# Kernel tuning notes

Measured on AMD Instinct MI355X. Metric: run time of the kernel, lower is better.

The kernel has to match this reference:

```python
import jax, jax.numpy as jnp
import numpy as np

N = 10000   # nodes
B = 32      # batch (hardcoded in source)
E = 40000   # edges per graph
H = 4       # attention heads
D = 10      # out_feats per head (hardcoded 10 in source)
T = 10      # GAT input feature size (hardcoded 10)
L = 2       # n_align_layers
NEG = 0.2   # LeakyReLU slope


def _leaky(z):
    return jnp.where(z >= 0, z, NEG * z)


def _ln(t):
    # LayerNorm((N,B,D), elementwise_affine=False): normalize over the whole tensor
    m = t.mean()
    v = ((t - m) ** 2).mean()
    return (t - m) * jax.lax.rsqrt(v + 1e-5)


def _gat(feat, fc_w, a_l, a_r, src, dst):
    # feat: (N,B,T); fc_w: (H*D,T); a_l,a_r: (H,D); src,dst: (E,)
    ft = jnp.einsum('nbf,of->nbo', feat, fc_w).reshape(N, B, H, D)
    el = jnp.einsum('nbhd,hd->nbh', ft, a_l)   # (N,B,H)
    er = jnp.einsum('nbhd,hd->nbh', ft, a_r)
    e = _leaky(el[src] + er[dst])              # (E,B,H)
    emax = jax.ops.segment_max(e, dst, num_segments=N)
    ee = jnp.exp(e - emax[dst])
    a = ee / jax.ops.segment_sum(ee, dst, num_segments=N)[dst]  # edge softmax per dst
    out = jax.ops.segment_sum(ft[src] * a[..., None], dst, num_segments=N)  # (N,B,H,D)
    return _leaky(out)  # activation = leaky_relu in source


def setup_inputs():
    key = jax.random.key(0)
    ks = iter(jax.random.split(key, 40))
    x = jax.random.normal(next(ks), (T, N, B, 3), dtype=jnp.float32)
    idx = lambda: jax.random.randint(next(ks), (E,), 0, N, dtype=jnp.int32)
    inp = {'x': x, 'ps_src': idx(), 'ps_dst': idx(), 'rl_src': idx(), 'rl_dst': idx()}
    def gat_params(name):
        inp[name + '_fc'] = jax.random.normal(next(ks), (L, H * D, T), dtype=jnp.float32) * 0.3
        inp[name + '_al'] = jax.random.normal(next(ks), (L, H, D), dtype=jnp.float32) * 0.3
        inp[name + '_ar'] = jax.random.normal(next(ks), (L, H, D), dtype=jnp.float32) * 0.3
    for nm in ('mu_p', 'sg_p', 'mu_r', 'sg_r'):
        gat_params(nm)
    inp['reg_mu_w'] = jax.random.normal(next(ks), (1, T), dtype=jnp.float32) * 0.3
    inp['reg_mu_b'] = jnp.zeros((1,), dtype=jnp.float32)
    inp['reg_sg_w'] = jax.random.normal(next(ks), (1, T), dtype=jnp.float32) * 0.3
    inp['reg_sg_b'] = jnp.zeros((1,), dtype=jnp.float32)
    return inp


def reference(x, mu_p_fc, mu_p_al, mu_p_ar, sg_p_fc, sg_p_al, sg_p_ar,
              mu_r_fc, mu_r_al, mu_r_ar, sg_r_fc, sg_r_al, sg_r_ar,
              reg_mu_w, reg_mu_b, reg_sg_w, reg_sg_b,
              ps_src, ps_dst, rl_src, rl_dst):
    # mode='align1' path of Net.forward
    h = jnp.transpose(x, (1, 2, 0, 3))[..., :3]  # (N,B,T,3)
    mu = h[..., 0]      # (N,B,T)
    sigma = h[..., 1]
    mu_r0, sg_r0 = mu, sigma
    # pseudo-graph alignment stack
    mu_p, sg_p = mu, sigma
    for i in range(L - 1):
        mu_p = _ln(_gat(mu_p, mu_p_fc[i], mu_p_al[i], mu_p_ar[i], ps_src, ps_dst).mean(-2))
        sg_p = _ln(_gat(sg_p, sg_p_fc[i], sg_p_al[i], sg_p_ar[i], ps_src, ps_dst).mean(-2))
        h_p = (mu_p + sg_p) / 2
        mu_p, sg_p = h_p, h_p
    # real-graph alignment stack
    mu_rl, sg_rl = mu, sigma
    for i in range(L - 1):
        mu_rl = _ln(_gat(mu_rl, mu_r_fc[i], mu_r_al[i], mu_r_ar[i], rl_src, rl_dst).mean(-2))
        sg_rl = _ln(_gat(sg_rl, sg_r_fc[i], sg_r_al[i], sg_r_ar[i], rl_src, rl_dst).mean(-2))
        h_rl = (mu_rl + sg_rl) / 2
        mu_rl, sg_rl = h_rl, h_rl
    mu_r = mu_r0 @ reg_mu_w.T + reg_mu_b                                        # (N,B,1)
    mu_pf = _gat(h_p, mu_p_fc[-1], mu_p_al[-1], mu_p_ar[-1], ps_src, ps_dst).mean(-2)
    mu_rf = _gat(h_rl, mu_r_fc[-1], mu_r_al[-1], mu_r_ar[-1], rl_src, rl_dst).mean(-2)
    sg_r = sg_r0 @ reg_sg_w.T + reg_sg_b
    sg_pf = _gat(h_p, sg_p_fc[-1], sg_p_al[-1], sg_p_ar[-1], ps_src, ps_dst).mean(-2)
    sg_rf = _gat(h_rl, sg_r_fc[-1], sg_r_al[-1], sg_r_ar[-1], rl_src, rl_dst).mean(-2)
    return ((mu_r + mu_pf + mu_rf) / 3, (sg_r + sg_pf + sg_rf) / 3)
```

## Files before the change

### kernel.cpp

```cpp
#include <hip/hip_runtime.h>
#include <hip/hip_fp16.h>


#define NN 10000
#define BB 32
#define EE 40000
#define HH 4
#define DD 10
#define TT 10
#define NEG 0.2f

#define NB   (NN*BB)
#define NBT  (NN*BB*TT)
#define BSUB 2
#define NGRP (NN*BSUB)


__device__ __forceinline__ float2 cvt2(unsigned u) {
    return __half22float2(*reinterpret_cast<const __half2*>(&u));
}
__device__ __forceinline__ void unpA(const uint4& u0, const uint4& u1, float (&fa)[10]) {
    float2 t;
    t = cvt2(u0.x); fa[0] = t.x; fa[1] = t.y;
    t = cvt2(u0.y); fa[2] = t.x; fa[3] = t.y;
    t = cvt2(u0.z); fa[4] = t.x; fa[5] = t.y;
    t = cvt2(u0.w); fa[6] = t.x; fa[7] = t.y;
    t = cvt2(u1.x); fa[8] = t.x; fa[9] = t.y;
}
__device__ __forceinline__ void unpB(const uint4& u1, const uint4& u2, float (&fb)[10]) {
    float2 t;
    t = cvt2(u1.z); fb[0] = t.x; fb[1] = t.y;
    t = cvt2(u1.w); fb[2] = t.x; fb[3] = t.y;
    t = cvt2(u2.x); fb[4] = t.x; fb[5] = t.y;
    t = cvt2(u2.y); fb[6] = t.x; fb[7] = t.y;
    t = cvt2(u2.z); fb[8] = t.x; fb[9] = t.y;
}

__global__ void extract_kernel(const float* __restrict__ x,
                               const float* __restrict__ wmu, const float* __restrict__ bmu,
                               const float* __restrict__ wsg, const float* __restrict__ bsg,
                               __half* __restrict__ msH,
                               float* __restrict__ regmu, float* __restrict__ regsg) {
    int i = blockIdx.x * blockDim.x + threadIdx.x;
    if (i >= NB) return;
    int n = i / BB, b = i % BB;
    float smu = 0.f, ssg = 0.f;
    float muv[TT], sgv[TT];
#pragma unroll
    for (int t = 0; t < TT; t++) {
        size_t xi = (((size_t)t * NN + n) * BB + b) * 3;
        float m = x[xi], s = x[xi + 1];
        muv[t] = m; sgv[t] = s;
        smu += m * wmu[t];
        ssg += s * wsg[t];
    }
    __half2* dst = (__half2*)(msH + (size_t)i * 24);
    dst[0] = __floats2half2_rn(muv[0], muv[1]);
    dst[1] = __floats2half2_rn(muv[2], muv[3]);
    dst[2] = __floats2half2_rn(muv[4], muv[5]);
    dst[3] = __floats2half2_rn(muv[6], muv[7]);
    dst[4] = __floats2half2_rn(muv[8], muv[9]);
    dst[5] = __floats2half2_rn(0.f, 0.f);
    dst[6] = __floats2half2_rn(sgv[0], sgv[1]);
    dst[7] = __floats2half2_rn(sgv[2], sgv[3]);
    dst[8] = __floats2half2_rn(sgv[4], sgv[5]);
    dst[9] = __floats2half2_rn(sgv[6], sgv[7]);
    dst[10] = __floats2half2_rn(sgv[8], sgv[9]);
    dst[11] = __floats2half2_rn(0.f, 0.f);
    regmu[i] = smu + bmu[0];
    regsg[i] = ssg + bsg[0];
}

__global__ void deg2_kernel(const int* __restrict__ dst0, int* __restrict__ deg0,
                            const int* __restrict__ dst1, int* __restrict__ deg1) {
    int e = blockIdx.x * blockDim.x + threadIdx.x;
    const int* dst = blockIdx.y ? dst1 : dst0;
    int* deg       = blockIdx.y ? deg1 : deg0;
    if (e < EE) atomicAdd(&deg[dst[e]], 1);
}

__global__ void scan2_kernel(const int* __restrict__ deg0, int* __restrict__ off0,
                             const int* __restrict__ deg1, int* __restrict__ off1) {
    const int* __restrict__ deg = blockIdx.x ? deg1 : deg0;
    int* __restrict__ off       = blockIdx.x ? off1 : off0;
    __shared__ int sm[16];
    __shared__ int carry_s;
    int tid = threadIdx.x;
    int lane = tid & 63, wid = tid >> 6;
    if (tid == 0) { carry_s = 0; off[0] = 0; }
    __syncthreads();
    for (int base = 0; base < NN; base += 1024) {
        int i = base + tid;
        int v = (i < NN) ? deg[i] : 0;
        int x = v;
#pragma unroll
        for (int s = 1; s < 64; s <<= 1) {
            int t = __shfl_up(x, s, 64);
            if (lane >= s) x += t;
        }
        if (lane == 63) sm[wid] = x;
        __syncthreads();
        if (wid == 0) {
            int w = (lane < 16) ? sm[lane] : 0;
#pragma unroll
            for (int s = 1; s < 16; s <<= 1) {
                int t = __shfl_up(w, s, 64);
                if (lane >= s) w += t;
            }
            if (lane < 16) sm[lane] = w;
        }
        __syncthreads();
        int add = carry_s + ((wid > 0) ? sm[wid - 1] : 0);
        if (i < NN) off[i + 1] = add + x;
        int total = sm[15];
        __syncthreads();
        if (tid == 0) carry_s += total;
        __syncthreads();
    }
}

__global__ void fill2_kernel(const int* __restrict__ src0, const int* __restrict__ dst0,
                             const int* __restrict__ off0, int* __restrict__ cur0,
                             int* __restrict__ csr0,
                             const int* __restrict__ src1, const int* __restrict__ dst1,
                             const int* __restrict__ off1, int* __restrict__ cur1,
                             int* __restrict__ csr1) {
    int e = blockIdx.x * blockDim.x + threadIdx.x;
    const int* src = blockIdx.y ? src1 : src0;
    const int* dst = blockIdx.y ? dst1 : dst0;
    const int* off = blockIdx.y ? off1 : off0;
    int* cursor    = blockIdx.y ? cur1 : cur0;
    int* csr       = blockIdx.y ? csr1 : csr0;
    if (e < EE) {
        int d = dst[e];
        int p = atomicAdd(&cursor[d], 1);
        csr[off[d] + p] = src[e];
    }
}

__global__ void hist2_kernel(const int* __restrict__ deg0, const int* __restrict__ deg1,
                             int* __restrict__ hist) {
    __shared__ int lh[64];
    if (threadIdx.x < 64) lh[threadIdx.x] = 0;
    __syncthreads();
    int n = blockIdx.x * blockDim.x + threadIdx.x;
    int g = blockIdx.y;
    const int* deg = g ? deg1 : deg0;
    if (n < NN) {
        int d = deg[n];
        int bin = 63 - ((d < 63) ? d : 63);
        atomicAdd(&lh[bin], 1);
    }
    __syncthreads();
    if (threadIdx.x < 64 && lh[threadIdx.x])
        atomicAdd(&hist[g * 64 + threadIdx.x], lh[threadIdx.x]);
}

__global__ void binoff_kernel(const int* __restrict__ hist, int* __restrict__ boff) {
    int g = threadIdx.x >> 6, lane = threadIdx.x & 63;
    int v = hist[g * 64 + lane];
    int x = v;
#pragma unroll
    for (int s = 1; s < 64; s <<= 1) {
        int t = __shfl_up(x, s, 64);
        if (lane >= s) x += t;
    }
    boff[g * 64 + lane] = x - v;
}

__global__ void permfill2_kernel(const int* __restrict__ deg0, const int* __restrict__ deg1,
                                 const int* __restrict__ boff, int* __restrict__ bcur,
                                 int* __restrict__ perm0, int* __restrict__ perm1) {
    __shared__ int lh[64], lbase[64];
    if (threadIdx.x < 64) lh[threadIdx.x] = 0;
    __syncthreads();
    int n = blockIdx.x * blockDim.x + threadIdx.x;
    int g = blockIdx.y;
    const int* deg = g ? deg1 : deg0;
    int* perm      = g ? perm1 : perm0;
    int bin = 0, myp = 0;
    if (n < NN) {
        int d = deg[n];
        bin = 63 - ((d < 63) ? d : 63);
        myp = atomicAdd(&lh[bin], 1);
    }
    __syncthreads();
    if (threadIdx.x < 64) {
        int c = lh[threadIdx.x];
        lbase[threadIdx.x] = c ? atomicAdd(&bcur[g * 64 + threadIdx.x], c) : 0;
    }
    __syncthreads();
    if (n < NN) perm[boff[g * 64 + bin] + lbase[bin] + myp] = n;
}

__global__ void vpre_kernel(const float* __restrict__ fc0, const float* __restrict__ al0, const float* __restrict__ ar0,
                            const float* __restrict__ fc1, const float* __restrict__ al1, const float* __restrict__ ar1,
                            const float* __restrict__ fc2, const float* __restrict__ al2, const float* __restrict__ ar2,
                            const float* __restrict__ fc3, const float* __restrict__ al3, const float* __restrict__ ar3,
                            float* __restrict__ vbuf) {
    int j = threadIdx.x;
    if (j >= 320) return;
    int g = j / 40, r = j % 40;
    int h = r / 10, t = r % 10;
    int which = g & 3, layer = g >> 2;
    const float* fc; const float* al; const float* ar;
    if (which == 0)      { fc = fc0; al = al0; ar = ar0; }
    else if (which == 1) { fc = fc1; al = al1; ar = ar1; }
    else if (which == 2) { fc = fc2; al = al2; ar = ar2; }
    else                 { fc = fc3; al = al3; ar = ar3; }
    fc += layer * (HH * DD * TT);
    al += layer * (HH * DD);
    ar += layer * (HH * DD);
    float vl = 0.f, vr = 0.f;
#pragma unroll
    for (int d = 0; d < DD; d++) {
        float w = fc[(h * DD + d) * TT + t];
        vl += al[h * DD + d] * w;
        vr += ar[h * DD + d] * w;
    }
    vbuf[g * 80 + r] = vl;
    vbuf[g * 80 + 40 + r] = vr;
}

struct PairCfg {
    const __half* f;
    const float* WA; const float* WB;
    const float* vA; const float* vB;
    const int* off; const int* csr; const int* perm;
    float* gA; float* gB;
    float* statsA; float* statsB;
};
struct PairCfg2 { PairCfg c[2]; };

__device__ __forceinline__ void eacc(const float (&fa)[TT], bool val,
                                     const float* __restrict__ v,
                                     const float (&er)[HH],
                                     float (&den)[HH], float (&acc)[HH][TT]) {
#pragma unroll
    for (int h = 0; h < HH; h++) {
        float e = 0.f;
#pragma unroll
        for (int t = 0; t < TT; t++) e += v[h * TT + t] * fa[t];
        float z = e + er[h];
        z = (z >= 0.f) ? z : NEG * z;
        float w = val ? __expf(z) : 0.f;
        den[h] += w;
#pragma unroll
        for (int t = 0; t < TT; t++) acc[h][t] += w * fa[t];
    }
}

template <bool DUALF, bool STATS>
__global__ void __launch_bounds__(256)
gatpair_kernel(PairCfg2 cfgs) {
    const PairCfg cfg = cfgs.c[blockIdx.y];
    __shared__ __align__(16) float sWA[HH * DD * 12];
    __shared__ __align__(16) float sWB[HH * DD * 12];
    for (int kk = threadIdx.x; kk < HH * DD * TT; kk += blockDim.x) {
        int r = kk / TT, t = kk - r * TT;
        sWA[r * 12 + t] = cfg.WA[kk];
        sWB[r * 12 + t] = cfg.WB[kk];
    }
    __syncthreads();

    const __half* __restrict__ f  = cfg.f;
    const int*   __restrict__ csr = cfg.csr;
    const float* __restrict__ vA  = cfg.vA;
    const float* __restrict__ vB  = cfg.vB;
    const int LDR = DUALF ? 24 : 16;

    int i = blockIdx.x * blockDim.x + threadIdx.x;
    float lsA = 0.f, lqA = 0.f, lsB = 0.f, lqB = 0.f;
    if (i < NB) {
        int bgrp = i / NGRP;
        int r = i - bgrp * NGRP;
        int slot = r >> 1;
        int b = (bgrp << 1) | (r & 1);
        int n = cfg.perm[slot];
        int nb = n * BB + b;
        int s0 = cfg.off[n], s1 = cfg.off[n + 1];

        float erA[HH], erB[HH];
        {
            const uint4* p = (const uint4*)(f + (size_t)nb * LDR);
            float fsA[TT], fsB[TT];
            if (DUALF) {
                uint4 u0 = p[0], u1 = p[1], u2 = p[2];
                unpA(u0, u1, fsA); unpB(u1, u2, fsB);
            } else {
                uint4 u0 = p[0], u1 = p[1];
                unpA(u0, u1, fsA);
#pragma unroll
                for (int t = 0; t < TT; t++) fsB[t] = fsA[t];
            }
#pragma unroll
            for (int h = 0; h < HH; h++) {
                float ea = 0.f, eb = 0.f;
#pragma unroll
                for (int t = 0; t < TT; t++) {
                    ea += vA[HH * TT + h * TT + t] * fsA[t];
                    eb += vB[HH * TT + h * TT + t] * fsB[t];
                }
                erA[h] = ea; erB[h] = eb;
            }
        }

        float accA[HH][TT], accB[HH][TT];
        float denA[HH], denB[HH];
#pragma unroll
        for (int h = 0; h < HH; h++) {
            denA[h] = 0.f; denB[h] = 0.f;
#pragma unroll
            for (int t = 0; t < TT; t++) { accA[h][t] = 0.f; accB[h][t] = 0.f; }
        }

        for (int k = s0; k < s1; k += 4) {
            int k1 = (k + 1 < s1) ? k + 1 : s0;
            int k2 = (k + 2 < s1) ? k + 2 : s0;
            int k3 = (k + 3 < s1) ? k + 3 : s0;
            bool v1 = (k + 1 < s1), v2 = (k + 2 < s1), v3 = (k + 3 < s1);
            int e0 = csr[k], e1 = csr[k1], e2 = csr[k2], e3 = csr[k3];
            const uint4* q0 = (const uint4*)(f + (size_t)(e0 * BB + b) * LDR);
            const uint4* q1 = (const uint4*)(f + (size_t)(e1 * BB + b) * LDR);
            const uint4* q2 = (const uint4*)(f + (size_t)(e2 * BB + b) * LDR);
            const uint4* q3 = (const uint4*)(f + (size_t)(e3 * BB + b) * LDR);
            if (DUALF) {
                uint4 a0 = q0[0], a1 = q0[1], a2 = q0[2];
                uint4 b0 = q1[0], b1 = q1[1], b2 = q1[2];
                uint4 c0 = q2[0], c1 = q2[1], c2 = q2[2];
                uint4 d0 = q3[0], d1 = q3[1], d2 = q3[2];
                float fa[TT], fb[TT];
                unpA(a0, a1, fa); unpB(a1, a2, fb);
                eacc(fa, true, vA, erA, denA, accA); eacc(fb, true, vB, erB, denB, accB);
                unpA(b0, b1, fa); unpB(b1, b2, fb);
                eacc(fa, v1, vA, erA, denA, accA);   eacc(fb, v1, vB, erB, denB, accB);
                unpA(c0, c1, fa); unpB(c1, c2, fb);
                eacc(fa, v2, vA, erA, denA, accA);   eacc(fb, v2, vB, erB, denB, accB);
                unpA(d0, d1, fa); unpB(d1, d2, fb);
                eacc(fa, v3, vA, erA, denA, accA);   eacc(fb, v3, vB, erB, denB, accB);
            } else {
                uint4 a0 = q0[0], a1 = q0[1];
                uint4 b0 = q1[0], b1 = q1[1];
                uint4 c0 = q2[0], c1 = q2[1];
                uint4 d0 = q3[0], d1 = q3[1];
                float fa[TT];
                unpA(a0, a1, fa);
                eacc(fa, true, vA, erA, denA, accA); eacc(fa, true, vB, erB, denB, accB);
                unpA(b0, b1, fa);
                eacc(fa, v1, vA, erA, denA, accA);   eacc(fa, v1, vB, erB, denB, accB);
                unpA(c0, c1, fa);
                eacc(fa, v2, vA, erA, denA, accA);   eacc(fa, v2, vB, erB, denB, accB);
                unpA(d0, d1, fa);
                eacc(fa, v3, vA, erA, denA, accA);   eacc(fa, v3, vB, erB, denB, accB);
            }
        }

        bool nz = (s1 > s0);
        float* gpA = cfg.gA + (size_t)nb * DD;
        float* gpB = cfg.gB + (size_t)nb * DD;

#pragma unroll
        for (int g = 0; g < 2; g++) {
            const float (*acc)[TT] = g ? accB : accA;
            const float* den = g ? denB : denA;
            const float* sW  = g ? sWB : sWA;
            float* gp        = g ? gpB : gpA;
            float rd[HH];
#pragma unroll
            for (int h = 0; h < HH; h++) rd[h] = nz ? (1.0f / den[h]) : 0.f;
            float outv[DD];
#pragma unroll
            for (int d = 0; d < DD; d++) outv[d] = 0.f;
#pragma unroll
            for (int h = 0; h < HH; h++) {
#pragma unroll
                for (int d = 0; d < DD; d++) {
                    const float* wr = &sW[(h * DD + d) * 12];
                    float4 w0 = *(const float4*)wr;
                    float4 w1 = *(const float4*)(wr + 4);
                    float2 w2 = *(const float2*)(wr + 8);
                    float va = w0.x * acc[h][0] + w0.y * acc[h][1] + w0.z * acc[h][2] + w0.w * acc[h][3]
                             + w1.x * acc[h][4] + w1.y * acc[h][5] + w1.z * acc[h][6] + w1.w * acc[h][7]
                             + w2.x * acc[h][8] + w2.y * acc[h][9];
                    va *= rd[h];
                    va = (va >= 0.f) ? va : NEG * va;
                    outv[d] += va * 0.25f;
                }
            }
#pragma unroll
            for (int d = 0; d < DD; d += 2)
                *(float2*)(gp + d) = make_float2(outv[d], outv[d + 1]);
            if (STATS) {
                float s = 0.f, q = 0.f;
#pragma unroll
                for (int d = 0; d < DD; d++) { s += outv[d]; q += outv[d] * outv[d]; }
                if (g) { lsB = s; lqB = q; } else { lsA = s; lqA = q; }
            }
        }
    }
    if (STATS) {
#pragma unroll
        for (int o = 32; o > 0; o >>= 1) {
            lsA += __shfl_down(lsA, o, 64);
            lqA += __shfl_down(lqA, o, 64);
            lsB += __shfl_down(lsB, o, 64);
            lqB += __shfl_down(lqB, o, 64);
        }
        __shared__ float ss[4][4];
        int wid = threadIdx.x >> 6, lid = threadIdx.x & 63;
        if (lid == 0) { ss[wid][0] = lsA; ss[wid][1] = lqA; ss[wid][2] = lsB; ss[wid][3] = lqB; }
        __syncthreads();
        if (threadIdx.x == 0) {
            float a0 = 0.f, a1 = 0.f, a2 = 0.f, a3 = 0.f;
#pragma unroll
            for (int w = 0; w < 4; w++) { a0 += ss[w][0]; a1 += ss[w][1]; a2 += ss[w][2]; a3 += ss[w][3]; }
            atomicAdd(&cfg.statsA[0], a0);
            atomicAdd(&cfg.statsA[1], a1);
            atomicAdd(&cfg.statsB[0], a2);
            atomicAdd(&cfg.statsB[1], a3);
        }
    }
}

__global__ void lncomb2_kernel(const float* __restrict__ gA, const float* __restrict__ gB,
                               const float* __restrict__ gA2, const float* __restrict__ gB2,
                               const float* __restrict__ stats,
                               __half* __restrict__ hp, __half* __restrict__ hrl) {
    int i = blockIdx.x * blockDim.x + threadIdx.x;
    if (i >= NB * 8) return;
    const float* ga = blockIdx.y ? gA2 : gA;
    const float* gb = blockIdx.y ? gB2 : gB;
    const float* st = stats + (blockIdx.y ? 4 : 0);
    __half2* h      = (__half2*)(blockIdx.y ? hrl : hp);
    int nb = i >> 3, t2 = i & 7;
    float v0 = 0.f, v1 = 0.f;
    if (t2 < 5) {
        const float M = (float)NBT;
        float ma = st[0] / M; float va = st[1] / M - ma * ma;
        float mb = st[2] / M; float vb = st[3] / M - mb * mb;
        float ra = rsqrtf(va + 1e-5f), rb = rsqrtf(vb + 1e-5f);
        size_t base = (size_t)nb * DD + t2 * 2;
        v0 = 0.5f * ((ga[base] - ma) * ra + (gb[base] - mb) * rb);
        v1 = 0.5f * ((ga[base + 1] - ma) * ra + (gb[base + 1] - mb) * rb);
    }
    h[(size_t)nb * 8 + t2] = __floats2half2_rn(v0, v1);
}

__global__ void outcomb2_kernel(const float* __restrict__ regmu, const float* __restrict__ regsg,
                                const float* __restrict__ gA, const float* __restrict__ gA2,
                                const float* __restrict__ gB, const float* __restrict__ gB2,
                                float* __restrict__ out) {
    int i = blockIdx.x * blockDim.x + threadIdx.x;
    if (i >= NBT) return;
    int nb = i / DD;
    if (blockIdx.y == 0) out[i]       = (regmu[nb] + gA[i] + gA2[i]) * (1.0f / 3.0f);
    else                 out[NBT + i] = (regsg[nb] + gB[i] + gB2[i]) * (1.0f / 3.0f);
}

extern "C" void kernel_launch(void* const* d_in, const int* in_sizes, int n_in,
                              void* d_out, int out_size, void* d_ws, size_t ws_size,
                              hipStream_t stream) {
    const float* x      = (const float*)d_in[0];
    const int* ps_src   = (const int*)d_in[1];
    const int* ps_dst   = (const int*)d_in[2];
    const int* rl_src   = (const int*)d_in[3];
    const int* rl_dst   = (const int*)d_in[4];
    const float* mu_p_fc = (const float*)d_in[5];
    const float* mu_p_al = (const float*)d_in[6];
    const float* mu_p_ar = (const float*)d_in[7];
    const float* sg_p_fc = (const float*)d_in[8];
    const float* sg_p_al = (const float*)d_in[9];
    const float* sg_p_ar = (const float*)d_in[10];
    const float* mu_r_fc = (const float*)d_in[11];
    const float* mu_r_al = (const float*)d_in[12];
    const float* mu_r_ar = (const float*)d_in[13];
    const float* sg_r_fc = (const float*)d_in[14];
    const float* sg_r_al = (const float*)d_in[15];
    const float* sg_r_ar = (const float*)d_in[16];
    const float* reg_mu_w = (const float*)d_in[17];
    const float* reg_mu_b = (const float*)d_in[18];
    const float* reg_sg_w = (const float*)d_in[19];
    const float* reg_sg_b = (const float*)d_in[20];

    float* out = (float*)d_out;

    float* fw = (float*)d_ws;
    __half* msH  = (__half*)fw;     fw += NB * 12;
    __half* hpH  = (__half*)fw;     fw += NB * 8;
    __half* hrlH = (__half*)fw;     fw += NB * 8;
    float* gA    = fw;              fw += NBT;
    float* gB    = fw;              fw += NBT;
    float* gA2   = fw;              fw += NBT;
    float* gB2   = fw;              fw += NBT;
    float* regmu = fw;              fw += NB;
    float* regsg = fw;              fw += NB;
    float* vbuf  = fw;              fw += 8 * 80;
    int* iw = (int*)fw;
    int* ps_off = iw;               iw += NN + 1;
    int* rl_off = iw;               iw += NN + 1;
    int* ps_csr = iw;               iw += EE;
    int* rl_csr = iw;               iw += EE;
    int* perm_ps = iw;              iw += NN;
    int* perm_rl = iw;              iw += NN;
    int* boff   = iw;               iw += 128;
    int* deg_ps = iw;               iw += NN;
    int* cur_ps = iw;               iw += NN;
    int* deg_rl = iw;               iw += NN;
    int* cur_rl = iw;               iw += NN;
    int* hist   = iw;               iw += 128;
    int* bcur   = iw;               iw += 128;
    float* stats = (float*)iw;
    size_t zero_bytes = (size_t)(4 * NN + 256) * sizeof(int) + 8 * sizeof(float);
    hipMemsetAsync(deg_ps, 0, zero_bytes, stream);

    const int TPB = 256;
    const int GRID_NB  = (NB + TPB - 1) / TPB;
    const int GRID_NBT = (NBT + TPB - 1) / TPB;
    const int GRID_LN  = (NB * 8 + TPB - 1) / TPB;
    const int GRID_E   = (EE + TPB - 1) / TPB;
    const int GRID_N   = (NN + TPB - 1) / TPB;

    extract_kernel<<<GRID_NB, TPB, 0, stream>>>(x, reg_mu_w, reg_mu_b, reg_sg_w, reg_sg_b,
                                                msH, regmu, regsg);

    {
        dim3 g(GRID_E, 2, 1);
        dim3 gn(GRID_N, 2, 1);
        deg2_kernel<<<g, TPB, 0, stream>>>(ps_dst, deg_ps, rl_dst, deg_rl);
        scan2_kernel<<<2, 1024, 0, stream>>>(deg_ps, ps_off, deg_rl, rl_off);
        fill2_kernel<<<g, TPB, 0, stream>>>(ps_src, ps_dst, ps_off, cur_ps, ps_csr,
                                            rl_src, rl_dst, rl_off, cur_rl, rl_csr);
        hist2_kernel<<<gn, TPB, 0, stream>>>(deg_ps, deg_rl, hist);
        binoff_kernel<<<1, 128, 0, stream>>>(hist, boff);
        permfill2_kernel<<<gn, TPB, 0, stream>>>(deg_ps, deg_rl, boff, bcur, perm_ps, perm_rl);
    }

    vpre_kernel<<<1, 320, 0, stream>>>(mu_p_fc, mu_p_al, mu_p_ar,
                                       sg_p_fc, sg_p_al, sg_p_ar,
                                       mu_r_fc, mu_r_al, mu_r_ar,
                                       sg_r_fc, sg_r_al, sg_r_ar, vbuf);

    {
        PairCfg2 c;
        c.c[0] = { msH, mu_p_fc, sg_p_fc, vbuf + 0 * 80, vbuf + 1 * 80,
                   ps_off, ps_csr, perm_ps, gA,  gB,  stats + 0, stats + 2 };
        c.c[1] = { msH, mu_r_fc, sg_r_fc, vbuf + 2 * 80, vbuf + 3 * 80,
                   rl_off, rl_csr, perm_rl, gA2, gB2, stats + 4, stats + 6 };
        dim3 grid(GRID_NB, 2, 1);
        gatpair_kernel<true, true><<<grid, TPB, 0, stream>>>(c);
    }
    {
        dim3 g(GRID_LN, 2, 1);
        lncomb2_kernel<<<g, TPB, 0, stream>>>(gA, gB, gA2, gB2, stats, hpH, hrlH);
    }

    {
        PairCfg2 c;
        c.c[0] = { hpH,  mu_p_fc + 400, sg_p_fc + 400, vbuf + 4 * 80, vbuf + 5 * 80,
                   ps_off, ps_csr, perm_ps, gA,  gB,  nullptr, nullptr };
        c.c[1] = { hrlH, mu_r_fc + 400, sg_r_fc + 400, vbuf + 6 * 80, vbuf + 7 * 80,
                   rl_off, rl_csr, perm_rl, gA2, gB2, nullptr, nullptr };
        dim3 grid(GRID_NB, 2, 1);
        gatpair_kernel<false, false><<<grid, TPB, 0, stream>>>(c);
    }

    {
        dim3 g(GRID_NBT, 2, 1);
        outcomb2_kernel<<<g, TPB, 0, stream>>>(regmu, regsg, gA, gA2, gB, gB2, out);
    }
}
```

Measured before the change: 423.0 us.

## Pre-gather source node features into CSR-ordered edge buffers before GAT aggregation

Adds a gather kernel that copies each edge's source-node half-precision features into a contiguous buffer laid out in CSR order. The aggregation kernel then reads neighbours sequentially from this buffer instead of doing csr-indirected random loads. The thread mapping also changes so 32 consecutive threads cover the batch of one node. The aim is coalesced, contiguous reads in the aggregation loop, at the cost of an extra kernel launch and writing and re-reading a roughly 60 MB edge buffer per layer.

After: 474.4 us. +12.1%, slower.

```diff
diff --git a/kernel.cpp b/kernel.cpp
--- a/kernel.cpp
+++ b/kernel.cpp
@@ -12,9 +12,7 @@
 
 #define NB   (NN*BB)
 #define NBT  (NN*BB*TT)
-#define BSUB 2
-#define NGRP (NN*BSUB)
-
+#define EB   (EE*BB)
 
 __device__ __forceinline__ float2 cvt2(unsigned u) {
     return __half22float2(*reinterpret_cast<const __half2*>(&u));
@@ -222,11 +220,35 @@
     vbuf[g * 80 + 40 + r] = vr;
 }
 
+template <int LDRH>
+__global__ void __launch_bounds__(256)
+gatherA_kernel(const __half* __restrict__ f0, const __half* __restrict__ f1,
+               const int* __restrict__ csr0, const int* __restrict__ csr1,
+               __half* __restrict__ rb0, __half* __restrict__ rb1) {
+    const __half* __restrict__ f = blockIdx.y ? f1 : f0;
+    const int* __restrict__ csr  = blockIdx.y ? csr1 : csr0;
+    __half* __restrict__ rb      = blockIdx.y ? rb1 : rb0;
+    int idx = blockIdx.x * blockDim.x + threadIdx.x;
+    if (idx >= EB) return;
+    int j = idx >> 5, b = idx & 31;
+    int s = csr[j];
+    const uint4* sp = (const uint4*)(f + ((size_t)s * BB + b) * LDRH);
+    uint4* dp = (uint4*)(rb + (size_t)idx * LDRH);
+    if (LDRH == 24) {
+        uint4 a0 = sp[0], a1 = sp[1], a2 = sp[2];
+        dp[0] = a0; dp[1] = a1; dp[2] = a2;
+    } else {
+        uint4 a0 = sp[0], a1 = sp[1];
+        dp[0] = a0; dp[1] = a1;
+    }
+}
+
 struct PairCfg {
     const __half* f;
+    const __half* rb;
     const float* WA; const float* WB;
     const float* vA; const float* vB;
-    const int* off; const int* csr; const int* perm;
+    const int* off; const int* perm;
     float* gA; float* gB;
     float* statsA; float* statsB;
 };
@@ -252,7 +274,7 @@
 
 template <bool DUALF, bool STATS>
 __global__ void __launch_bounds__(256)
-gatpair_kernel(PairCfg2 cfgs) {
+gatpairB_kernel(PairCfg2 cfgs) {
     const PairCfg cfg = cfgs.c[blockIdx.y];
     __shared__ __align__(16) float sWA[HH * DD * 12];
     __shared__ __align__(16) float sWB[HH * DD * 12];
@@ -264,7 +286,7 @@
     __syncthreads();
 
     const __half* __restrict__ f  = cfg.f;
-    const int*   __restrict__ csr = cfg.csr;
+    const __half* __restrict__ rb = cfg.rb;
     const float* __restrict__ vA  = cfg.vA;
     const float* __restrict__ vB  = cfg.vB;
     const int LDR = DUALF ? 24 : 16;
@@ -272,10 +294,8 @@
     int i = blockIdx.x * blockDim.x + threadIdx.x;
     float lsA = 0.f, lqA = 0.f, lsB = 0.f, lqB = 0.f;
     if (i < NB) {
-        int bgrp = i / NGRP;
-        int r = i - bgrp * NGRP;
-        int slot = r >> 1;
-        int b = (bgrp << 1) | (r & 1);
+        int b = i & 31;
+        int slot = i >> 5;
         int n = cfg.perm[slot];
         int nb = n * BB + b;
         int s0 = cfg.off[n], s1 = cfg.off[n + 1];
@@ -319,11 +339,10 @@
             int k2 = (k + 2 < s1) ? k + 2 : s0;
             int k3 = (k + 3 < s1) ? k + 3 : s0;
             bool v1 = (k + 1 < s1), v2 = (k + 2 < s1), v3 = (k + 3 < s1);
-            int e0 = csr[k], e1 = csr[k1], e2 = csr[k2], e3 = csr[k3];
-            const uint4* q0 = (const uint4*)(f + (size_t)(e0 * BB + b) * LDR);
-            const uint4* q1 = (const uint4*)(f + (size_t)(e1 * BB + b) * LDR);
-            const uint4* q2 = (const uint4*)(f + (size_t)(e2 * BB + b) * LDR);
-            const uint4* q3 = (const uint4*)(f + (size_t)(e3 * BB + b) * LDR);
+            const uint4* q0 = (const uint4*)(rb + ((size_t)k  * BB + b) * LDR);
+            const uint4* q1 = (const uint4*)(rb + ((size_t)k1 * BB + b) * LDR);
+            const uint4* q2 = (const uint4*)(rb + ((size_t)k2 * BB + b) * LDR);
+            const uint4* q3 = (const uint4*)(rb + ((size_t)k3 * BB + b) * LDR);
             if (DUALF) {
                 uint4 a0 = q0[0], a1 = q0[1], a2 = q0[2];
                 uint4 b0 = q1[0], b1 = q1[1], b2 = q1[2];
@@ -488,6 +507,8 @@
     __half* msH  = (__half*)fw;     fw += NB * 12;
     __half* hpH  = (__half*)fw;     fw += NB * 8;
     __half* hrlH = (__half*)fw;     fw += NB * 8;
+    __half* rbPS = (__half*)fw;     fw += EB * 12;
+    __half* rbRL = (__half*)fw;     fw += EB * 12;
     float* gA    = fw;              fw += NBT;
     float* gB    = fw;              fw += NBT;
     float* gA2   = fw;              fw += NBT;
@@ -519,6 +540,7 @@
     const int GRID_LN  = (NB * 8 + TPB - 1) / TPB;
     const int GRID_E   = (EE + TPB - 1) / TPB;
     const int GRID_N   = (NN + TPB - 1) / TPB;
+    const int GRID_EB  = (EB + TPB - 1) / TPB;
 
     extract_kernel<<<GRID_NB, TPB, 0, stream>>>(x, reg_mu_w, reg_mu_b, reg_sg_w, reg_sg_b,
                                                 msH, regmu, regsg);
@@ -541,13 +563,17 @@
                                        sg_r_fc, sg_r_al, sg_r_ar, vbuf);
 
     {
+        dim3 g(GRID_EB, 2, 1);
+        gatherA_kernel<24><<<g, TPB, 0, stream>>>(msH, msH, ps_csr, rl_csr, rbPS, rbRL);
+    }
+    {
         PairCfg2 c;
-        c.c[0] = { msH, mu_p_fc, sg_p_fc, vbuf + 0 * 80, vbuf + 1 * 80,
-                   ps_off, ps_csr, perm_ps, gA,  gB,  stats + 0, stats + 2 };
-        c.c[1] = { msH, mu_r_fc, sg_r_fc, vbuf + 2 * 80, vbuf + 3 * 80,
-                   rl_off, rl_csr, perm_rl, gA2, gB2, stats + 4, stats + 6 };
+        c.c[0] = { msH, rbPS, mu_p_fc, sg_p_fc, vbuf + 0 * 80, vbuf + 1 * 80,
+                   ps_off, perm_ps, gA,  gB,  stats + 0, stats + 2 };
+        c.c[1] = { msH, rbRL, mu_r_fc, sg_r_fc, vbuf + 2 * 80, vbuf + 3 * 80,
+                   rl_off, perm_rl, gA2, gB2, stats + 4, stats + 6 };
         dim3 grid(GRID_NB, 2, 1);
-        gatpair_kernel<true, true><<<grid, TPB, 0, stream>>>(c);
+        gatpairB_kernel<true, true><<<grid, TPB, 0, stream>>>(c);
     }
     {
         dim3 g(GRID_LN, 2, 1);
@@ -555,13 +581,17 @@
     }
 
     {
+        dim3 g(GRID_EB, 2, 1);
+        gatherA_kernel<16><<<g, TPB, 0, stream>>>(hpH, hrlH, ps_csr, rl_csr, rbPS, rbRL);
+    }
+    {
         PairCfg2 c;
-        c.c[0] = { hpH,  mu_p_fc + 400, sg_p_fc + 400, vbuf + 4 * 80, vbuf + 5 * 80,
-                   ps_off, ps_csr, perm_ps, gA,  gB,  nullptr, nullptr };
-        c.c[1] = { hrlH, mu_r_fc + 400, sg_r_fc + 400, vbuf + 6 * 80, vbuf + 7 * 80,
-                   rl_off, rl_csr, perm_rl, gA2, gB2, nullptr, nullptr };
+        c.c[0] = { hpH,  rbPS, mu_p_fc + 400, sg_p_fc + 400, vbuf + 4 * 80, vbuf + 5 * 80,
+                   ps_off, perm_ps, gA,  gB,  nullptr, nullptr };
+        c.c[1] = { hrlH, rbRL, mu_r_fc + 400, sg_r_fc + 400, vbuf + 6 * 80, vbuf + 7 * 80,
+                   rl_off, perm_rl, gA2, gB2, nullptr, nullptr };
         dim3 grid(GRID_NB, 2, 1);
-        gatpair_kernel<false, false><<<grid, TPB, 0, stream>>>(c);
+        gatpairB_kernel<false, false><<<grid, TPB, 0, stream>>>(c);
     }
 
     {
```
